# Kernel tuning notes

Hardware: AMD Instinct MI355X
Metric: run time of the kernel (lower is better)

The kernel has to match this reference:

```python
import jax, jax.numpy as jnp
import numpy as np

E, C, FE, FS, K = 8, 1024, 1024, 4096, 2  # n_experts, embed, expert_inter, shared_inter, top_k
B, T = 4, 2048

def setup_inputs() -> dict:
    key = jax.random.key(0)
    ks = jax.random.split(key, 8)
    def init(k, shape, fan_in):
        return jax.random.normal(k, shape, jnp.float32) / np.sqrt(fan_in).astype(np.float32)
    return dict(
        x=jax.random.normal(ks[0], (B, T, C), jnp.float32),
        gate_w=init(ks[1], (E, C), C),        # nn.Linear(C, E, bias=False).weight
        ew1=init(ks[2], (E, C, FE), C),       # per-expert ln1 weights (transposed)
        ew2=init(ks[3], (E, C, FE), C),       # per-expert ln2 weights
        ewp=init(ks[4], (E, FE, C), FE),      # per-expert proj weights
        sw1=init(ks[5], (C, FS), C),          # shared FFN ln1
        sw2=init(ks[6], (C, FS), C),          # shared FFN ln2
        swp=init(ks[7], (FS, C), FS),         # shared FFN proj
    )

def reference(x, gate_w, ew1, ew2, ewp, sw1, sw2, swp):
    Bd, Td, Cd = x.shape
    xf = x.reshape(-1, Cd)                               # [N, C]
    scores = xf @ gate_w.T                               # [N, E] (eval mode: no noise)
    probs = jax.nn.softmax(scores, axis=-1)
    weights, indices = jax.lax.top_k(probs, K)           # [N, K]
    N = xf.shape[0]
    # combine[n, e] = routing weight of expert e for token n (0 if not selected)
    combine = jnp.zeros((N, E), xf.dtype).at[jnp.arange(N)[:, None], indices].add(weights)
    y = jnp.zeros_like(xf)
    for i in range(E):  # fixed small expert count; masked-dense replaces torch gather/scatter
        h = jax.nn.silu(xf @ ew1[i]) * (xf @ ew2[i])     # [N, FE] SwiGLU
        y = y + (h @ ewp[i]) * combine[:, i:i + 1]
    z = (jax.nn.silu(xf @ sw1) * (xf @ sw2)) @ swp       # shared expert (dropout p=0)
    return (y + z).reshape(Bd, Td, Cd), scores
```

## Files before the change

kernel.cpp:

```cpp
#include <hip/hip_runtime.h>

typedef unsigned short u16;
typedef unsigned int u32;
typedef __bf16 bf16x8 __attribute__((ext_vector_type(8)));
typedef float f32x4 __attribute__((ext_vector_type(4)));
typedef u16 u16x8 __attribute__((ext_vector_type(8)));

#define NTOK 8192
#define CDIM 1024
#define NEXP 8
#define FEDIM 1024
#define FSDIM 4096

#define GLD16(gp, lp) __builtin_amdgcn_global_load_lds( \
    (const __attribute__((address_space(1))) void*)(gp), \
    (__attribute__((address_space(3))) void*)(lp), 16, 0, 0)

__device__ __forceinline__ u16 f2bf(float f) {
  u32 u = __float_as_uint(f);
  u += 0x7FFFu + ((u >> 16) & 1u);
  return (u16)(u >> 16);
}

__global__ __launch_bounds__(256) void gate_kernel(
    const float* __restrict__ x, const float* __restrict__ gw,
    float* __restrict__ scores, u16* __restrict__ xb, int* __restrict__ cnt,
    int* __restrict__ tok, float* __restrict__ wgt)
{
  __shared__ int lcnt[NEXP];
  __shared__ int lbase[NEXP];
  __shared__ int rec_i[32];
  __shared__ int rec_p1[32], rec_p2[32];
  __shared__ float rec_w1[32], rec_w2[32];

  int tid = threadIdx.x, wave = tid >> 6, lane = tid & 63;
  if (tid < NEXP) lcnt[tid] = 0;
  __syncthreads();

  int tbase = blockIdx.x * 32 + wave * 8;
#pragma unroll
  for (int it = 0; it < 8; ++it) {
    int n = tbase + it;
    const float4* xr = (const float4*)(x + (size_t)n * CDIM) + lane * 4;
    float4 xv[4];
#pragma unroll
    for (int j = 0; j < 4; j++) xv[j] = xr[j];
    u16x8 rA, rB;
    rA[0]=f2bf(xv[0].x); rA[1]=f2bf(xv[0].y); rA[2]=f2bf(xv[0].z); rA[3]=f2bf(xv[0].w);
    rA[4]=f2bf(xv[1].x); rA[5]=f2bf(xv[1].y); rA[6]=f2bf(xv[1].z); rA[7]=f2bf(xv[1].w);
    rB[0]=f2bf(xv[2].x); rB[1]=f2bf(xv[2].y); rB[2]=f2bf(xv[2].z); rB[3]=f2bf(xv[2].w);
    rB[4]=f2bf(xv[3].x); rB[5]=f2bf(xv[3].y); rB[6]=f2bf(xv[3].z); rB[7]=f2bf(xv[3].w);
    u16* xrow = xb + (size_t)n * CDIM + lane * 16;
    *(u16x8*)xrow = rA;
    *(u16x8*)(xrow + 8) = rB;

    float s[NEXP];
#pragma unroll
    for (int e = 0; e < NEXP; e++) {
      const float4* g = (const float4*)(gw + (size_t)e * CDIM) + lane * 4;
      float a = 0.f;
#pragma unroll
      for (int j = 0; j < 4; j++) {
        float4 gv = g[j];
        a += xv[j].x * gv.x + xv[j].y * gv.y + xv[j].z * gv.z + xv[j].w * gv.w;
      }
#pragma unroll
      for (int o = 32; o > 0; o >>= 1) a += __shfl_xor(a, o);
      s[e] = a;
    }
    if (lane == 0) {
      float m = s[0];
      for (int e = 1; e < NEXP; e++) m = fmaxf(m, s[e]);
      float p[NEXP], sum = 0.f;
      for (int e = 0; e < NEXP; e++) { p[e] = __expf(s[e] - m); sum += p[e]; }
      int i1 = 0;
      for (int e = 1; e < NEXP; e++) if (p[e] > p[i1]) i1 = e;
      int i2 = (i1 == 0) ? 1 : 0;
      for (int e = 0; e < NEXP; e++) if (e != i1 && p[e] > p[i2]) i2 = e;
      float w1 = p[i1] / sum, w2 = p[i2] / sum;
#pragma unroll
      for (int e = 0; e < NEXP; e++) scores[(size_t)n * NEXP + e] = s[e];
      int p1 = atomicAdd(&lcnt[i1], 1);
      int p2 = atomicAdd(&lcnt[i2], 1);
      int slot = wave * 8 + it;
      rec_i[slot] = i1 | (i2 << 8);
      rec_p1[slot] = p1; rec_p2[slot] = p2;
      rec_w1[slot] = w1; rec_w2[slot] = w2;
    }
  }
  __syncthreads();
  if (tid < NEXP) lbase[tid] = atomicAdd(&cnt[tid], lcnt[tid]);
  __syncthreads();
  if (tid < 32) {
    int n = blockIdx.x * 32 + tid;
    int i1 = rec_i[tid] & 0xff, i2 = rec_i[tid] >> 8;
    int q1 = lbase[i1] + rec_p1[tid];
    int q2 = lbase[i2] + rec_p2[tid];
    tok[i1 * NTOK + q1] = n; wgt[i1 * NTOK + q1] = rec_w1[tid];
    tok[i2 * NTOK + q2] = n; wgt[i2 * NTOK + q2] = rec_w2[tid];
  }
}

__global__ void prefix_kernel(const int* __restrict__ cnt, int* __restrict__ prefix) {
  if (threadIdx.x == 0 && blockIdx.x == 0) {
    int a = 0;
    for (int e = 0; e < NEXP; e++) { prefix[e] = a; a += cnt[e]; }
    prefix[NEXP] = a;
  }
}

__global__ __launch_bounds__(256) void transpose_kernel(const float* __restrict__ src,
    u16* __restrict__ dst, int R, int C)
{
  __shared__ float tile[32][33];
  size_t base = (size_t)blockIdx.z * R * C;
  int c0 = blockIdx.x * 32, r0 = blockIdx.y * 32;
  int tx = threadIdx.x & 31, ty = threadIdx.x >> 5;
#pragma unroll
  for (int i = 0; i < 4; i++) {
    int r = ty + i * 8;
    tile[r][tx] = src[base + (size_t)(r0 + r) * C + c0 + tx];
  }
  __syncthreads();
#pragma unroll
  for (int i = 0; i < 4; i++) {
    int c = ty + i * 8;
    dst[base + (size_t)(c0 + c) * R + r0 + tx] = f2bf(tile[tx][c]);
  }
}

__global__ __launch_bounds__(256) void transpose_i_kernel(
    const float* __restrict__ s1, const float* __restrict__ s2,
    u16* __restrict__ dst, int R, int C, size_t sstride, size_t dstride)
{
  __shared__ float t1[32][33], t2[32][33];
  size_t sbase = (size_t)blockIdx.z * sstride;
  size_t dbase = (size_t)blockIdx.z * dstride;
  int c0 = blockIdx.x * 32, r0 = blockIdx.y * 32;
  int tx = threadIdx.x & 31, ty = threadIdx.x >> 5;
#pragma unroll
  for (int i = 0; i < 4; i++) {
    int r = ty + i * 8;
    t1[r][tx] = s1[sbase + (size_t)(r0 + r) * C + c0 + tx];
    t2[r][tx] = s2[sbase + (size_t)(r0 + r) * C + c0 + tx];
  }
  __syncthreads();
#pragma unroll
  for (int i = 0; i < 4; i++) {
    int c = ty + i * 8;
    dst[dbase + (size_t)(2 * (c0 + c) + 0) * R + r0 + tx] = f2bf(t1[tx][c]);
    dst[dbase + (size_t)(2 * (c0 + c) + 1) * R + r0 + tx] = f2bf(t2[tx][c]);
  }
}

#define BM2 256
#define BK2 64

template<int EPI, int AMODE, int BN_>
__global__ __launch_bounds__(512, 2) void gemm256(
    const u16* __restrict__ A, int lda,
    const u16* __restrict__ B, size_t bstride, int ldb,
    int M, int K,
    u16* __restrict__ Hout, int ldh,
    float* __restrict__ outF, int ldo,
    const int* __restrict__ cnt, const int* __restrict__ prefix,
    const int* __restrict__ tok, const float* __restrict__ wgt)
{
  constexpr int WN = BN_ / 4;
  constexpr int N_REP = WN / 16;
  constexpr int ACH = 4;
  constexpr int BCH = BN_ / 64;

  int e = blockIdx.z;
  int Mloc = (AMODE == 0) ? M : cnt[e];
  int mbase = blockIdx.y * BM2;
  if (AMODE != 0 && mbase >= Mloc) return;
  int nbase = blockIdx.x * BN_;
  int tid = threadIdx.x;
  int lane = tid & 63;
  int wid = tid >> 6;
  int wr = wid >> 2, wc = wid & 3;
  int fr = lane & 15;

  __shared__ __align__(16) u16 As[2][BM2 * BK2];
  __shared__ __align__(16) u16 Bs[2][BN_ * BK2];

  int srow = tid >> 3;
  int scol = ((tid & 7) ^ (srow & 7)) * 8;
  int pfx = (AMODE == 0) ? 0 : prefix[e];

  size_t arow[ACH];
#pragma unroll
  for (int c = 0; c < ACH; c++) {
    int rloc = mbase + c * 64 + srow;
    if (AMODE == 0)      arow[c] = rloc;
    else if (AMODE == 1) arow[c] = tok[e * NTOK + min(rloc, Mloc - 1)];
    else                 arow[c] = pfx + min(rloc, Mloc - 1);
  }
  const u16* Aps[ACH];
#pragma unroll
  for (int c = 0; c < ACH; c++) Aps[c] = A + arow[c] * (size_t)lda + scol;
  const u16* Bb = B + ((AMODE != 0) ? (size_t)e * bstride : 0);
  const u16* Bps[BCH];
#pragma unroll
  for (int c = 0; c < BCH; c++)
    Bps[c] = Bb + (size_t)(nbase + c * 64 + srow) * ldb + scol;

  auto STAGE = [&](int buf, int kof) {
#pragma unroll
    for (int c = 0; c < ACH; c++) GLD16(Aps[c] + kof, &As[buf][c * 4096 + tid * 8]);
#pragma unroll
    for (int c = 0; c < BCH; c++) GLD16(Bps[c] + kof, &Bs[buf][c * 4096 + tid * 8]);
  };

  f32x4 acc[8][N_REP] = {};

  int nt = K / BK2;
  STAGE(0, 0);
  asm volatile("s_waitcnt vmcnt(0)" ::: "memory");
  __builtin_amdgcn_s_barrier();
  __builtin_amdgcn_sched_barrier(0);

  int slot0 = (((lane >> 4)) ^ (fr & 7)) << 3;
  int slot1 = ((4 + (lane >> 4)) ^ (fr & 7)) << 3;

  for (int t = 0; t < nt; ++t) {
    int c = t & 1;
    bool pf = (t + 1 < nt);
    const u16* asb = &As[c][(wr * 128 + fr) * BK2];
    const u16* bsb = &Bs[c][(wc * WN + fr) * BK2];

    bf16x8 b0[N_REP], a0[4];
#pragma unroll
    for (int n = 0; n < N_REP; n++) b0[n] = *(const bf16x8*)&bsb[n * 1024 + slot0];
#pragma unroll
    for (int m = 0; m < 4; m++) a0[m] = *(const bf16x8*)&asb[m * 1024 + slot0];
    if (pf) STAGE(c ^ 1, (t + 1) * BK2);
    __builtin_amdgcn_s_barrier();
    asm volatile("s_waitcnt lgkmcnt(0)" ::: "memory");
    __builtin_amdgcn_sched_barrier(0);
    __builtin_amdgcn_s_setprio(1);
#pragma unroll
    for (int m = 0; m < 4; m++)
#pragma unroll
      for (int n = 0; n < N_REP; n++)
        acc[m][n] = __builtin_amdgcn_mfma_f32_16x16x32_bf16(a0[m], b0[n], acc[m][n], 0, 0, 0);
    __builtin_amdgcn_s_setprio(0);
    __builtin_amdgcn_s_barrier();
    __builtin_amdgcn_sched_barrier(0);

    bf16x8 a1[4];
#pragma unroll
    for (int m = 0; m < 4; m++) a1[m] = *(const bf16x8*)&asb[(4 + m) * 1024 + slot0];
    __builtin_amdgcn_s_barrier();
    asm volatile("s_waitcnt lgkmcnt(0)" ::: "memory");
    __builtin_amdgcn_sched_barrier(0);
    __builtin_amdgcn_s_setprio(1);
#pragma unroll
    for (int m = 0; m < 4; m++)
#pragma unroll
      for (int n = 0; n < N_REP; n++)
        acc[4 + m][n] = __builtin_amdgcn_mfma_f32_16x16x32_bf16(a1[m], b0[n], acc[4 + m][n], 0, 0, 0);
    __builtin_amdgcn_s_setprio(0);
    __builtin_amdgcn_s_barrier();
    __builtin_amdgcn_sched_barrier(0);

    bf16x8 b1[N_REP], a2[4];
#pragma unroll
    for (int n = 0; n < N_REP; n++) b1[n] = *(const bf16x8*)&bsb[n * 1024 + slot1];
#pragma unroll
    for (int m = 0; m < 4; m++) a2[m] = *(const bf16x8*)&asb[(4 + m) * 1024 + slot1];
    __builtin_amdgcn_s_barrier();
    asm volatile("s_waitcnt lgkmcnt(0)" ::: "memory");
    __builtin_amdgcn_sched_barrier(0);
    __builtin_amdgcn_s_setprio(1);
#pragma unroll
    for (int m = 0; m < 4; m++)
#pragma unroll
      for (int n = 0; n < N_REP; n++)
        acc[4 + m][n] = __builtin_amdgcn_mfma_f32_16x16x32_bf16(a2[m], b1[n], acc[4 + m][n], 0, 0, 0);
    __builtin_amdgcn_s_setprio(0);
    __builtin_amdgcn_s_barrier();
    __builtin_amdgcn_sched_barrier(0);

    bf16x8 a3[4];
#pragma unroll
    for (int m = 0; m < 4; m++) a3[m] = *(const bf16x8*)&asb[m * 1024 + slot1];
    __builtin_amdgcn_s_barrier();
    asm volatile("s_waitcnt lgkmcnt(0)" ::: "memory");
    __builtin_amdgcn_sched_barrier(0);
    __builtin_amdgcn_s_setprio(1);
#pragma unroll
    for (int m = 0; m < 4; m++)
#pragma unroll
      for (int n = 0; n < N_REP; n++)
        acc[m][n] = __builtin_amdgcn_mfma_f32_16x16x32_bf16(a3[m], b1[n], acc[m][n], 0, 0, 0);
    __builtin_amdgcn_s_setprio(0);
    if (pf) asm volatile("s_waitcnt vmcnt(0)" ::: "memory");
    __builtin_amdgcn_s_barrier();
    __builtin_amdgcn_sched_barrier(0);
  }

#pragma unroll
  for (int m = 0; m < 8; m++) {
#pragma unroll
    for (int j = 0; j < 4; j++) {
      int rloc = wr * 128 + m * 16 + (lane >> 4) * 4 + j;
      int rr = mbase + rloc;
      if (AMODE != 0 && rr >= Mloc) continue;
      int tk = 0; float wv = 0.f;
      if (EPI == 4) { tk = tok[e * NTOK + rr]; wv = wgt[e * NTOK + rr]; }
#pragma unroll
      for (int n = 0; n < N_REP; n++) {
        int wcol = wc * WN + n * 16 + fr;
        float v = acc[m][n][j];
        if (EPI == 0) {
          float o = __shfl_xor(v, 1);
          float g  = (fr & 1) ? o : v;
          float vv = (fr & 1) ? v : o;
          float hv = (g / (1.f + __expf(-g))) * vv;
          if (!(fr & 1))
            Hout[(size_t)(pfx + rr) * ldh + ((nbase + wcol) >> 1)] = f2bf(hv);
        } else if (EPI == 2) {
          outF[(size_t)rr * ldo + nbase + wcol] = v;
        } else {
          unsafeAtomicAdd(&outF[(size_t)tk * ldo + nbase + wcol], v * wv);
        }
      }
    }
  }
}

extern "C" void kernel_launch(void* const* d_in, const int* in_sizes, int n_in,
                              void* d_out, int out_size, void* d_ws, size_t ws_size,
                              hipStream_t stream)
{
  const float* x   = (const float*)d_in[0];
  const float* gw  = (const float*)d_in[1];
  const float* ew1 = (const float*)d_in[2];
  const float* ew2 = (const float*)d_in[3];
  const float* ewp = (const float*)d_in[4];
  const float* sw1 = (const float*)d_in[5];
  const float* sw2 = (const float*)d_in[6];
  const float* swp = (const float*)d_in[7];
  float* out    = (float*)d_out;
  float* scores = out + (size_t)NTOK * CDIM;

  char* wsp = (char*)d_ws;
  size_t off = 0;
  auto alloc = [&](size_t bytes) -> void* {
    void* p = wsp + off; off += (bytes + 255) & ~(size_t)255; return p;
  };
  u16* xb   = (u16*)alloc((size_t)NTOK * CDIM * 2);
  u16* swi  = (u16*)alloc((size_t)2 * FSDIM * CDIM * 2);
  u16* ewi  = (u16*)alloc((size_t)NEXP * 2 * FEDIM * CDIM * 2);
  u16* swpt = (u16*)alloc((size_t)CDIM * FSDIM * 2);
  u16* ewpt = (u16*)alloc((size_t)NEXP * CDIM * FEDIM * 2);
  u16* hs   = (u16*)alloc((size_t)NTOK * FSDIM * 2);
  u16* he   = (u16*)alloc((size_t)2 * NTOK * FEDIM * 2);
  int* cnt  = (int*)alloc(256);
  int* pfx  = (int*)alloc(256);
  int* tok  = (int*)alloc((size_t)NEXP * NTOK * 4);
  float* wgt = (float*)alloc((size_t)NEXP * NTOK * 4);
  if (off > ws_size) return;

  hipMemsetAsync(cnt, 0, 32, stream);
  gate_kernel<<<NTOK / 32, 256, 0, stream>>>(x, gw, scores, xb, cnt, tok, wgt);
  prefix_kernel<<<1, 64, 0, stream>>>(cnt, pfx);
  transpose_i_kernel<<<dim3(FSDIM/32, CDIM/32, 1), 256, 0, stream>>>(
      sw1, sw2, swi, CDIM, FSDIM, 0, 0);
  transpose_i_kernel<<<dim3(FEDIM/32, CDIM/32, NEXP), 256, 0, stream>>>(
      ew1, ew2, ewi, CDIM, FEDIM, (size_t)CDIM * FEDIM, (size_t)2 * FEDIM * CDIM);
  transpose_kernel<<<dim3(CDIM/32, FSDIM/32, 1), 256, 0, stream>>>(swp, swpt, FSDIM, CDIM);
  transpose_kernel<<<dim3(CDIM/32, FEDIM/32, NEXP), 256, 0, stream>>>(ewp, ewpt, FEDIM, CDIM);

  gemm256<0,0,256><<<dim3(2*FSDIM/256, NTOK/256, 1), 512, 0, stream>>>(
      xb, CDIM, swi, 0, CDIM, NTOK, CDIM, hs, FSDIM, nullptr, 0,
      nullptr, nullptr, nullptr, nullptr);
  gemm256<2,0,128><<<dim3(CDIM/128, NTOK/256, 1), 512, 0, stream>>>(
      hs, FSDIM, swpt, 0, FSDIM, NTOK, FSDIM, nullptr, 0, out, CDIM,
      nullptr, nullptr, nullptr, nullptr);

  gemm256<0,1,256><<<dim3(2*FEDIM/256, NTOK/256, NEXP), 512, 0, stream>>>(
      xb, CDIM, ewi, (size_t)2 * FEDIM * CDIM, CDIM, 0, CDIM, he, FEDIM, nullptr, 0,
      cnt, pfx, tok, nullptr);
  gemm256<4,2,128><<<dim3(CDIM/128, NTOK/256, NEXP), 512, 0, stream>>>(
      he, FEDIM, ewpt, (size_t)CDIM * FEDIM, FEDIM, 0, FEDIM, nullptr, 0, out, CDIM,
      cnt, pfx, tok, wgt);
}
```

Measured before the change: 615.3 us.

## Interleave next-tile global-to-LDS loads across MFMA phases with partial vmcnt waits

The bulk prefetch of the next K tile is split into per-chunk loads. These are spread over the four MFMA phases of each iteration rather than issued all at once. Full `vmcnt(0)` drains are replaced by `vmcnt(2)`, so the A chunks needed only by the second half of the tile can stay in flight while the first half's MFMAs run. The aim is to smooth memory issue and hide load latency behind compute. The cost is more fragile ordering assumptions that depend on in-order vmcnt completion and on the chunk-to-row mapping.

```diff
diff --git a/kernel.cpp b/kernel.cpp
--- a/kernel.cpp
+++ b/kernel.cpp
@@ -206,18 +206,20 @@
   for (int c = 0; c < BCH; c++)
     Bps[c] = Bb + (size_t)(nbase + c * 64 + srow) * ldb + scol;
 
-  auto STAGE = [&](int buf, int kof) {
-#pragma unroll
-    for (int c = 0; c < ACH; c++) GLD16(Aps[c] + kof, &As[buf][c * 4096 + tid * 8]);
-#pragma unroll
-    for (int c = 0; c < BCH; c++) GLD16(Bps[c] + kof, &Bs[buf][c * 4096 + tid * 8]);
+  auto SA = [&](int buf, int ch, int kof) {
+    GLD16(Aps[ch] + kof, &As[buf][ch * 4096 + tid * 8]);
   };
+  auto SB = [&](int buf, int ch, int kof) {
+    GLD16(Bps[ch] + kof, &Bs[buf][ch * 4096 + tid * 8]);
+  };
 
   f32x4 acc[8][N_REP] = {};
 
   int nt = K / BK2;
-  STAGE(0, 0);
-  asm volatile("s_waitcnt vmcnt(0)" ::: "memory");
+#pragma unroll
+  for (int cb = 0; cb < BCH; cb++) SB(0, cb, 0);
+  SA(0, 0, 0); SA(0, 2, 0); SA(0, 1, 0); SA(0, 3, 0);
+  asm volatile("s_waitcnt vmcnt(2)" ::: "memory");
   __builtin_amdgcn_s_barrier();
   __builtin_amdgcn_sched_barrier(0);
 
@@ -225,8 +227,9 @@
   int slot1 = ((4 + (lane >> 4)) ^ (fr & 7)) << 3;
 
   for (int t = 0; t < nt; ++t) {
-    int c = t & 1;
+    int c = t & 1, o = c ^ 1;
     bool pf = (t + 1 < nt);
+    int kof = (t + 1) * BK2;
     const u16* asb = &As[c][(wr * 128 + fr) * BK2];
     const u16* bsb = &Bs[c][(wc * WN + fr) * BK2];
 
@@ -235,7 +238,7 @@
     for (int n = 0; n < N_REP; n++) b0[n] = *(const bf16x8*)&bsb[n * 1024 + slot0];
 #pragma unroll
     for (int m = 0; m < 4; m++) a0[m] = *(const bf16x8*)&asb[m * 1024 + slot0];
-    if (pf) STAGE(c ^ 1, (t + 1) * BK2);
+    if (pf) { SB(o, 0, kof); SB(o, 1, kof); }
     __builtin_amdgcn_s_barrier();
     asm volatile("s_waitcnt lgkmcnt(0)" ::: "memory");
     __builtin_amdgcn_sched_barrier(0);
@@ -246,12 +249,18 @@
       for (int n = 0; n < N_REP; n++)
         acc[m][n] = __builtin_amdgcn_mfma_f32_16x16x32_bf16(a0[m], b0[n], acc[m][n], 0, 0, 0);
     __builtin_amdgcn_s_setprio(0);
+    if (pf) asm volatile("s_waitcnt vmcnt(2)" ::: "memory");
+    else    asm volatile("s_waitcnt vmcnt(0)" ::: "memory");
     __builtin_amdgcn_s_barrier();
     __builtin_amdgcn_sched_barrier(0);
 
     bf16x8 a1[4];
 #pragma unroll
     for (int m = 0; m < 4; m++) a1[m] = *(const bf16x8*)&asb[(4 + m) * 1024 + slot0];
+    if (pf) {
+      if constexpr (BCH == 4) { SB(o, 2, kof); SB(o, 3, kof); }
+      else                    { SA(o, 0, kof); SA(o, 2, kof); }
+    }
     __builtin_amdgcn_s_barrier();
     asm volatile("s_waitcnt lgkmcnt(0)" ::: "memory");
     __builtin_amdgcn_sched_barrier(0);
@@ -270,6 +279,10 @@
     for (int n = 0; n < N_REP; n++) b1[n] = *(const bf16x8*)&bsb[n * 1024 + slot1];
 #pragma unroll
     for (int m = 0; m < 4; m++) a2[m] = *(const bf16x8*)&asb[(4 + m) * 1024 + slot1];
+    if (pf) {
+      if constexpr (BCH == 4) { SA(o, 0, kof); SA(o, 2, kof); }
+      else                    { SA(o, 1, kof); SA(o, 3, kof); }
+    }
     __builtin_amdgcn_s_barrier();
     asm volatile("s_waitcnt lgkmcnt(0)" ::: "memory");
     __builtin_amdgcn_sched_barrier(0);
@@ -286,6 +299,9 @@
     bf16x8 a3[4];
 #pragma unroll
     for (int m = 0; m < 4; m++) a3[m] = *(const bf16x8*)&asb[m * 1024 + slot1];
+    if (pf) {
+      if constexpr (BCH == 4) { SA(o, 1, kof); SA(o, 3, kof); }
+    }
     __builtin_amdgcn_s_barrier();
     asm volatile("s_waitcnt lgkmcnt(0)" ::: "memory");
     __builtin_amdgcn_sched_barrier(0);
@@ -296,7 +312,7 @@
       for (int n = 0; n < N_REP; n++)
         acc[m][n] = __builtin_amdgcn_mfma_f32_16x16x32_bf16(a3[m], b1[n], acc[m][n], 0, 0, 0);
     __builtin_amdgcn_s_setprio(0);
-    if (pf) asm volatile("s_waitcnt vmcnt(0)" ::: "memory");
+    if (pf) asm volatile("s_waitcnt vmcnt(2)" ::: "memory");
     __builtin_amdgcn_s_barrier();
     __builtin_amdgcn_sched_barrier(0);
   }
```

After: 615.9 us. Within noise of the previous version (+0.1%).
